# Kernel optimization log

Measured on AMD Instinct MI355X. Metric: run time of the kernel, lower is better.

The kernel has to match this reference:

```python
import jax, jax.numpy as jnp
import numpy as np

D = 8        # input_path_dim
S = 64       # cde_state_dim
H = 128      # vf_hidden_dim
OUT = 8      # output_path_dim
T = 2049     # time samples
B = 32       # batch (vmapped)
WIN = 16     # signature_window_size
NWIN = (T - 1) // WIN   # 128 scan steps
II, JJ = np.triu_indices(D, 1)    # Lyndon words of length 2: pairs i<j (P=28)


def setup_inputs() -> dict:
    key = jax.random.key(0)
    ks = jax.random.split(key, 16)
    g = lambda k, shp, fan: (jax.random.normal(k, shp, dtype=jnp.float32) / np.sqrt(fan)).astype(jnp.float32)
    z = lambda n: jnp.zeros((n,), jnp.float32)
    return {
        "ts": jnp.arange(T, dtype=jnp.float32),
        "x": jax.random.normal(ks[0], (B, T, D), dtype=jnp.float32) * 0.1,
        # initial MLP: d -> H -> H -> S, softplus activations
        "Wi0": g(ks[1], (H, D), D), "bi0": z(H),
        "Wi1": g(ks[2], (H, H), H), "bi1": z(H),
        "Wi2": g(ks[3], (S, H), H), "bi2": z(S),
        # vector-field MLP: S -> H -> H -> D*S, softplus hidden, tanh final
        "Wv0": g(ks[4], (H, S), S), "bv0": z(H),
        "Wv1": g(ks[5], (H, H), H), "bv1": z(H),
        "Wv2": g(ks[6], (D * S, H), H), "bv2": z(D * S),
        # readout: S -> OUT
        "Wr": g(ks[7], (OUT, S), S), "br": z(OUT),
    }


def _logsignatures(x):
    """Depth-2 log-signatures of a piecewise-linear path over windows.
    x: (B, T, D). Returns s1: (B, NWIN, D) increments, s2: (B, NWIN, P) Levy areas
    in the Lyndon basis [e_i, e_j], i<j."""
    delta = x[:, 1:] - x[:, :-1]                      # (B, T-1, D)
    delta = delta[:, : NWIN * WIN].reshape(x.shape[0], NWIN, WIN, D)
    s1 = delta.sum(axis=2)                            # (B, NWIN, D)
    cum = jnp.cumsum(delta, axis=2) - delta           # exclusive prefix sums
    M = jnp.einsum("bnwi,bnwj->bnij", cum, delta)    # (B, NWIN, D, D)
    L = 0.5 * (M - jnp.swapaxes(M, -1, -2))           # antisymmetric Levy area
    s2 = L[..., II, JJ]                               # (B, NWIN, P)
    return s1, s2


def reference(ts, x, Wi0, bi0, Wi1, bi1, Wi2, bi2, Wv0, bv0, Wv1, bv1, Wv2, bv2, Wr, br):
    sp = jax.nn.softplus

    def initial(x0):  # (D,) -> (S,)
        z = sp(Wi0 @ x0 + bi0)
        z = sp(Wi1 @ z + bi1)
        return Wi2 @ z + bi2

    def vf(h):  # (S,) -> (D, S): one vector field per input channel
        z = sp(Wv0 @ h + bv0)
        z = sp(Wv1 @ z + bv1)
        return jnp.tanh(Wv2 @ z + bv2).reshape(D, S)

    s1, s2 = _logsignatures(x)

    def single(x0_s, s1_s, s2_s):
        h0 = initial(x0_s)

        def step(h, sig):
            a, b = sig  # depth-1 (D,), depth-2 Lyndon coeffs (P,)
            V = vf(h)                          # (D, S)
            J = jax.jacfwd(vf)(h)              # (D, S, S) Jacobians dV_i/dh
            JV = jnp.einsum("dab,eb->dea", J, V)   # JV[j,i] = J_j @ V_i
            brack = JV[JJ, II] - JV[II, JJ]        # (P, S): [V_i, V_j], i<j
            hn = h + a @ V + b @ brack             # log-ODE step
            return hn, hn

        _, hist = jax.lax.scan(step, h0, (s1_s, s2_s))
        return jnp.concatenate([h0[None], hist], axis=0)   # (NWIN+1, S)

    hist = jax.vmap(single)(x[:, 0], s1, s2)    # (B, NWIN+1, S)
    return jnp.einsum("bns,os->bno", hist, Wr) + br   # evolving readout, identity act
```

## Files before the change

### kernel.cpp

```cpp
#include <hip/hip_runtime.h>
#include <hip/hip_bf16.h>

#define DD 8
#define SS 64
#define HH 128
#define OUTD 8
#define TT 2049
#define BB 32
#define WINW 16
#define NWIN 128
#define PP 28

typedef __attribute__((ext_vector_type(8))) short short8v;
typedef __attribute__((ext_vector_type(4))) float f32x4;

__device__ __forceinline__ float softplus_f(float x){
    return fmaxf(x, 0.f) + __logf(1.f + __expf(-fabsf(x)));
}
__device__ __forceinline__ float tanh_f(float x){
    float e = __expf(2.f * x);
    return 1.f - 2.f / (e + 1.f);
}
__device__ __forceinline__ void sp_sig(float x, float& sp, float& sg){
    float t = __expf(-fabsf(x));
    float r = 1.f / (1.f + t);
    sg = x > 0.f ? r : 1.f - r;
    sp = fmaxf(x, 0.f) - __logf(r);
}
__device__ __forceinline__ unsigned short f2bf(float f){
    return __builtin_bit_cast(unsigned short, __float2bfloat16(f));
}
__device__ __forceinline__ unsigned pk2(float a, float b){
    unsigned lo = (unsigned)__builtin_bit_cast(unsigned short, __float2bfloat16(a));
    unsigned hi = (unsigned)__builtin_bit_cast(unsigned short, __float2bfloat16(b));
    return lo | (hi << 16);
}

__global__ void sig_kernel(const float* __restrict__ x,
                           float* __restrict__ s1o, float* __restrict__ s2o){
    int w = blockIdx.x * blockDim.x + threadIdx.x;
    if (w >= BB * NWIN) return;
    int b = w >> 7, n = w & (NWIN - 1);
    const float* xp = x + ((size_t)b * TT + (size_t)n * WINW) * DD;
    float prev[DD], cum[DD], s1v[DD], M[DD][DD];
    #pragma unroll
    for (int i = 0; i < DD; ++i){
        cum[i] = 0.f; s1v[i] = 0.f;
        #pragma unroll
        for (int j = 0; j < DD; ++j) M[i][j] = 0.f;
    }
    #pragma unroll
    for (int i = 0; i < DD; ++i) prev[i] = xp[i];
    for (int t = 0; t < WINW; ++t){
        float cur[DD], del[DD];
        #pragma unroll
        for (int i = 0; i < DD; ++i) cur[i] = xp[(t + 1) * DD + i];
        #pragma unroll
        for (int i = 0; i < DD; ++i) del[i] = cur[i] - prev[i];
        #pragma unroll
        for (int i = 0; i < DD; ++i){
            #pragma unroll
            for (int j = 0; j < DD; ++j) M[i][j] += cum[i] * del[j];
        }
        #pragma unroll
        for (int i = 0; i < DD; ++i){ cum[i] += del[i]; s1v[i] += del[i]; prev[i] = cur[i]; }
    }
    #pragma unroll
    for (int i = 0; i < DD; ++i) s1o[(size_t)w * DD + i] = s1v[i];
    int p = 0;
    #pragma unroll
    for (int i = 0; i < DD; ++i){
        #pragma unroll
        for (int j = i + 1; j < DD; ++j){ s2o[(size_t)w * PP + p] = 0.5f * (M[i][j] - M[j][i]); ++p; }
    }
}

#define BPOS(k, nn) ((((k) >> 5) * 64 + (((k) >> 3) & 3) * 16 + (nn)) * 8 + ((k) & 7))

__global__ __launch_bounds__(512, 2) void scan_kernel(
    const float* __restrict__ x,
    const float* __restrict__ Wi0, const float* __restrict__ bi0,
    const float* __restrict__ Wi1, const float* __restrict__ bi1,
    const float* __restrict__ Wi2, const float* __restrict__ bi2,
    const float* __restrict__ Wv0, const float* __restrict__ bv0,
    const float* __restrict__ Wv1, const float* __restrict__ bv1,
    const float* __restrict__ Wv2, const float* __restrict__ bv2,
    const float* __restrict__ Wr,  const float* __restrict__ br,
    const float* __restrict__ s1g, const float* __restrict__ s2g,
    float* __restrict__ out)
{
    const int tid = threadIdx.x;
    const int w   = tid >> 6;
    const int l   = tid & 63;
    const int lg  = l >> 4;
    const int ln  = l & 15;
    const int b0  = blockIdx.x * 4;

    __shared__ __align__(16) short BpH[2 * 64 * 8];
    __shared__ __align__(16) short Bp0[4 * 64 * 8];
    __shared__ __align__(16) short Bp1[4 * 64 * 8];
    __shared__ __align__(16) short Bp7[2][2 * 64 * 8];
    __shared__ __align__(16) short Bp8[2][4 * 64 * 8];
    __shared__ __align__(16) short Bp9[2][4 * 64 * 8];
    __shared__ __align__(16) float s0p[4][HH], s1p[4][HH];
    __shared__ __align__(16) float Vl[4 * 512], Rf[4 * 512];
    __shared__ __align__(16) float hfb[4][2][SS];
    __shared__ __align__(16) float bv0L[HH], bv1L[HH], bv2L[512];
    __shared__ __align__(16) float WrL[OUTD * SS];
    __shared__ float brL[OUTD];
    __shared__ __align__(16) float sAll[4][NWIN * DD];
    __shared__ __align__(16) float bAll[4][NWIN * PP];
    __shared__ __align__(16) float outC[4][32][OUTD];
    __shared__ __align__(16) float Cexp[4][DD][12];

    short8v a0f[2], a1f[4];
    short8v a2f0[4], a2f1[4], a2f2[4], a2f3[4];
    #pragma unroll
    for (int ks = 0; ks < 2; ++ks){
        const float* p = Wv0 + (size_t)(w * 16 + ln) * SS + ks * 32 + lg * 8;
        short8v f;
        #pragma unroll
        for (int j = 0; j < 8; ++j) f[j] = (short)f2bf(p[j]);
        a0f[ks] = f;
    }
    #pragma unroll
    for (int ks = 0; ks < 4; ++ks){
        const float* p = Wv1 + (size_t)(w * 16 + ln) * HH + ks * 32 + lg * 8;
        short8v f;
        #pragma unroll
        for (int j = 0; j < 8; ++j) f[j] = (short)f2bf(p[j]);
        a1f[ks] = f;
    }
    #pragma unroll
    for (int ks = 0; ks < 4; ++ks){
        const float* p0 = Wv2 + (size_t)(64 * w + 0 * 16 + ln) * HH + ks * 32 + lg * 8;
        const float* p1 = Wv2 + (size_t)(64 * w + 1 * 16 + ln) * HH + ks * 32 + lg * 8;
        const float* p2 = Wv2 + (size_t)(64 * w + 2 * 16 + ln) * HH + ks * 32 + lg * 8;
        const float* p3 = Wv2 + (size_t)(64 * w + 3 * 16 + ln) * HH + ks * 32 + lg * 8;
        short8v f0, f1, f2, f3;
        #pragma unroll
        for (int j = 0; j < 8; ++j){
            f0[j] = (short)f2bf(p0[j]); f1[j] = (short)f2bf(p1[j]);
            f2[j] = (short)f2bf(p2[j]); f3[j] = (short)f2bf(p3[j]);
        }
        a2f0[ks] = f0; a2f1[ks] = f1; a2f2[ks] = f2; a2f3[ks] = f3;
    }
    if (tid < HH){ bv0L[tid] = bv0[tid]; bv1L[tid] = bv1[tid]; }
    bv2L[tid] = bv2[tid];
    WrL[tid]  = Wr[tid];
    if (tid < OUTD) brL[tid] = br[tid];
    {
        float* sF = &sAll[0][0];
        for (int i = tid; i < 4 * NWIN * DD; i += 512){
            int c = i >> 10;
            sF[i] = s1g[(size_t)(b0 + c) * (NWIN * DD) + (i & 1023)];
        }
        float* bF = &bAll[0][0];
        for (int i = tid; i < 4 * NWIN * PP; i += 512){
            int c = i / (NWIN * PP);
            bF[i] = s2g[(size_t)(b0 + c) * (NWIN * PP) + (i - c * (NWIN * PP))];
        }
        for (int i = tid; i < 2 * 64 * 8; i += 512) BpH[i] = 0;
        for (int i = tid; i < 4 * 64 * 8; i += 512){ Bp0[i] = 0; Bp1[i] = 0; }
    }
    __syncthreads();

    {
        int c4 = tid >> 7, r = tid & 127;
        float acc = bi0[r];
        const float* x0 = x + (size_t)(b0 + c4) * TT * DD;
        #pragma unroll
        for (int k = 0; k < DD; ++k) acc += Wi0[r * DD + k] * x0[k];
        s0p[c4][r] = softplus_f(acc);
    }
    if (tid < 256){
        int cc = tid >> 6, dd = (tid >> 3) & 7, ee = tid & 7;
        const float* bco = &bAll[cc][0];
        float cv = 0.f;
        if (ee < dd)      cv =  bco[((ee * (15 - ee)) >> 1) + dd - ee - 1];
        else if (ee > dd) cv = -bco[((dd * (15 - dd)) >> 1) + ee - dd - 1];
        Cexp[cc][dd][ee] = cv;
    }
    __syncthreads();
    {
        int c4 = tid >> 7, r = tid & 127;
        float acc = bi1[r];
        const f32x4* wv = (const f32x4*)(Wi1 + (size_t)r * HH);
        const f32x4* zv = (const f32x4*)&s0p[c4][0];
        #pragma unroll 8
        for (int k = 0; k < 32; ++k){
            f32x4 a = wv[k], z = zv[k];
            acc += a.x * z.x + a.y * z.y + a.z * z.z + a.w * z.w;
        }
        s1p[c4][r] = softplus_f(acc);
    }
    __syncthreads();
    if (tid < 256){
        int c4 = tid >> 6, s = tid & 63;
        float acc = bi2[s];
        const f32x4* wv = (const f32x4*)(Wi2 + (size_t)s * HH);
        const f32x4* zv = (const f32x4*)&s1p[c4][0];
        #pragma unroll 8
        for (int k = 0; k < 32; ++k){
            f32x4 a = wv[k], z = zv[k];
            acc += a.x * z.x + a.y * z.y + a.z * z.z + a.w * z.w;
        }
        hfb[c4][0][s] = acc;
        BpH[BPOS(s, c4)] = (short)f2bf(acc);
    }
    __syncthreads();

    const f32x4 zero4 = {0.f, 0.f, 0.f, 0.f};
    const int rb = w * 16 + lg * 4;

    for (int n = 0; n < NWIN; ++n){
        {
            f32x4 acc = zero4;
            acc = __builtin_amdgcn_mfma_f32_16x16x32_bf16(a0f[0], *(const short8v*)&BpH[(0 * 64 + l) * 8], acc, 0, 0, 0);
            acc = __builtin_amdgcn_mfma_f32_16x16x32_bf16(a0f[1], *(const short8v*)&BpH[(1 * 64 + l) * 8], acc, 0, 0, 0);
            if (ln < 4){
                int c = ln;
                f32x4 bv = *(const f32x4*)&bv0L[rb];
                float z[4], sgv[4];
                #pragma unroll
                for (int r = 0; r < 4; ++r){
                    float zz, gg;
                    sp_sig(acc[r] + bv[r], zz, gg);
                    z[r] = zz; sgv[r] = gg;
                }
                f32x4 sg = {sgv[0], sgv[1], sgv[2], sgv[3]};
                *(f32x4*)&s0p[c][rb] = sg;
                uint2 pk; pk.x = pk2(z[0], z[1]); pk.y = pk2(z[2], z[3]);
                *(uint2*)&Bp0[BPOS(rb, c)] = pk;
            }
        }
        __syncthreads();

        {
            f32x4 acc = zero4;
            #pragma unroll
            for (int ks = 0; ks < 4; ++ks)
                acc = __builtin_amdgcn_mfma_f32_16x16x32_bf16(a1f[ks], *(const short8v*)&Bp0[(ks * 64 + l) * 8], acc, 0, 0, 0);
            if (ln < 4){
                int c = ln;
                f32x4 bv = *(const f32x4*)&bv1L[rb];
                float z[4], sgv[4];
                #pragma unroll
                for (int r = 0; r < 4; ++r){
                    float zz, gg;
                    sp_sig(acc[r] + bv[r], zz, gg);
                    z[r] = zz; sgv[r] = gg;
                }
                f32x4 sg = {sgv[0], sgv[1], sgv[2], sgv[3]};
                *(f32x4*)&s1p[c][rb] = sg;
                uint2 pk; pk.x = pk2(z[0], z[1]); pk.y = pk2(z[2], z[3]);
                #pragma unroll
                for (int cc = 0; cc < 4; ++cc) *(uint2*)&Bp1[BPOS(rb, c * 4 + cc)] = pk;
            }
        }
        __syncthreads();

        {
            short8v bf[4];
            #pragma unroll
            for (int ks = 0; ks < 4; ++ks) bf[ks] = *(const short8v*)&Bp1[(ks * 64 + l) * 8];
            f32x4 acc0 = zero4, acc1 = zero4, acc2 = zero4, acc3 = zero4;
            #pragma unroll
            for (int ks = 0; ks < 4; ++ks){
                acc0 = __builtin_amdgcn_mfma_f32_16x16x32_bf16(a2f0[ks], bf[ks], acc0, 0, 0, 0);
                acc1 = __builtin_amdgcn_mfma_f32_16x16x32_bf16(a2f1[ks], bf[ks], acc1, 0, 0, 0);
                acc2 = __builtin_amdgcn_mfma_f32_16x16x32_bf16(a2f2[ks], bf[ks], acc2, 0, 0, 0);
                acc3 = __builtin_amdgcn_mfma_f32_16x16x32_bf16(a2f3[ks], bf[ks], acc3, 0, 0, 0);
            }
            {
                int c = ln >> 2, t = ln & 3;
                f32x4 av = (t == 0) ? acc0 : (t == 1) ? acc1 : (t == 2) ? acc2 : acc3;
                int r4 = 64 * w + t * 16 + lg * 4;
                f32x4 bv = *(const f32x4*)&bv2L[r4];
                f32x4 vv;
                #pragma unroll
                for (int r = 0; r < 4; ++r) vv[r] = tanh_f(av[r] + bv[r]);
                *(f32x4*)&Vl[c * 512 + r4] = vv;
            }
        }
        __syncthreads();

        {
            int c = tid >> 7, d = (tid >> 4) & 7, s0v = (tid & 15) * 4;
            f32x4 cm0 = *(const f32x4*)&Cexp[c][d][0];
            f32x4 cm1 = *(const f32x4*)&Cexp[c][d][4];
            f32x4 acc = zero4;
            #pragma unroll
            for (int e = 0; e < 8; ++e){
                float ce = (e < 4) ? cm0[e] : cm1[e - 4];
                f32x4 v4 = *(const f32x4*)&Vl[c * 512 + e * 64 + s0v];
                acc.x += ce * v4.x; acc.y += ce * v4.y;
                acc.z += ce * v4.z; acc.w += ce * v4.w;
            }
            uint2 pk; pk.x = pk2(acc.x, acc.y); pk.y = pk2(acc.z, acc.w);
            *(uint2*)&Bp7[c >> 1][BPOS(s0v, (c & 1) * 8 + d)] = pk;
        }
        __syncthreads();

        {
            #pragma unroll
            for (int p = 0; p < 2; ++p){
                f32x4 acc = zero4;
                acc = __builtin_amdgcn_mfma_f32_16x16x32_bf16(a0f[0], *(const short8v*)&Bp7[p][(0 * 64 + l) * 8], acc, 0, 0, 0);
                acc = __builtin_amdgcn_mfma_f32_16x16x32_bf16(a0f[1], *(const short8v*)&Bp7[p][(1 * 64 + l) * 8], acc, 0, 0, 0);
                int c = 2 * p + (ln >> 3);
                f32x4 sg = *(const f32x4*)&s0p[c][rb];
                uint2 pk; pk.x = pk2(sg[0] * acc[0], sg[1] * acc[1]);
                pk.y = pk2(sg[2] * acc[2], sg[3] * acc[3]);
                *(uint2*)&Bp8[p][BPOS(rb, ln)] = pk;
            }
        }
        __syncthreads();

        {
            #pragma unroll
            for (int p = 0; p < 2; ++p){
                f32x4 acc = zero4;
                #pragma unroll
                for (int ks = 0; ks < 4; ++ks)
                    acc = __builtin_amdgcn_mfma_f32_16x16x32_bf16(a1f[ks], *(const short8v*)&Bp8[p][(ks * 64 + l) * 8], acc, 0, 0, 0);
                int c = 2 * p + (ln >> 3), d = ln & 7;
                f32x4 sg = *(const f32x4*)&s1p[c][rb];
                uint2 pk; pk.x = pk2(sg[0] * acc[0], sg[1] * acc[1]);
                pk.y = pk2(sg[2] * acc[2], sg[3] * acc[3]);
                *(uint2*)&Bp9[d >> 2][BPOS(rb, (d & 3) * 4 + c)] = pk;
            }
        }
        __syncthreads();

        {
            const int im = w >> 2;
            short8v bf[4];
            #pragma unroll
            for (int ks = 0; ks < 4; ++ks) bf[ks] = *(const short8v*)&Bp9[im][(ks * 64 + l) * 8];
            f32x4 acc0 = zero4, acc1 = zero4, acc2 = zero4, acc3 = zero4;
            #pragma unroll
            for (int ks = 0; ks < 4; ++ks){
                acc0 = __builtin_amdgcn_mfma_f32_16x16x32_bf16(a2f0[ks], bf[ks], acc0, 0, 0, 0);
                acc1 = __builtin_amdgcn_mfma_f32_16x16x32_bf16(a2f1[ks], bf[ks], acc1, 0, 0, 0);
                acc2 = __builtin_amdgcn_mfma_f32_16x16x32_bf16(a2f2[ks], bf[ks], acc2, 0, 0, 0);
                acc3 = __builtin_amdgcn_mfma_f32_16x16x32_bf16(a2f3[ks], bf[ks], acc3, 0, 0, 0);
            }
            if ((ln >> 2) == (w & 3)){
                int c = ln & 3;
                #pragma unroll
                for (int t = 0; t < 4; ++t){
                    f32x4 av = (t == 0) ? acc0 : (t == 1) ? acc1 : (t == 2) ? acc2 : acc3;
                    int r4 = 64 * w + t * 16 + lg * 4;
                    f32x4 vv = *(const f32x4*)&Vl[c * 512 + r4];
                    f32x4 rr;
                    #pragma unroll
                    for (int r = 0; r < 4; ++r) rr[r] = (1.f - vv[r] * vv[r]) * av[r];
                    *(f32x4*)&Rf[c * 512 + r4] = rr;
                }
            }
        }
        __syncthreads();

        {
            const int cur = n & 1;
            if (w < 4){
                int c = w, s = l;
                f32x4 a0 = *(const f32x4*)&sAll[c][n * DD];
                f32x4 a1 = *(const f32x4*)&sAll[c][n * DD + 4];
                float hN = hfb[c][cur][s];
                #pragma unroll
                for (int d = 0; d < 4; ++d)
                    hN += a0[d] * Vl[c * 512 + d * 64 + s] + Rf[c * 512 + d * 64 + s];
                #pragma unroll
                for (int d = 4; d < 8; ++d)
                    hN += a1[d - 4] * Vl[c * 512 + d * 64 + s] + Rf[c * 512 + d * 64 + s];
                hfb[c][cur ^ 1][s] = hN;
                BpH[BPOS(s, c)] = (short)f2bf(hN);
            } else {
                {
                    int idx = (w - 4) * 64 + l;
                    int cc = idx >> 6, dd = (idx >> 3) & 7, ee = idx & 7;
                    int nn = (n + 1 < NWIN) ? n + 1 : NWIN - 1;
                    const float* bco = &bAll[cc][nn * PP];
                    float cv = 0.f;
                    if (ee < dd)      cv =  bco[((ee * (15 - ee)) >> 1) + dd - ee - 1];
                    else if (ee > dd) cv = -bco[((dd * (15 - dd)) >> 1) + ee - dd - 1];
                    Cexp[cc][dd][ee] = cv;
                }
                int c = w - 4;
                int o = l >> 3, qq = l & 7;
                f32x4 w0 = *(const f32x4*)&WrL[o * SS + qq * 8];
                f32x4 w1 = *(const f32x4*)&WrL[o * SS + qq * 8 + 4];
                f32x4 h0 = *(const f32x4*)&hfb[c][cur][qq * 8];
                f32x4 h1 = *(const f32x4*)&hfb[c][cur][qq * 8 + 4];
                float acc = w0.x*h0.x + w0.y*h0.y + w0.z*h0.z + w0.w*h0.w
                          + w1.x*h1.x + w1.y*h1.y + w1.z*h1.z + w1.w*h1.w;
                acc += __shfl_xor(acc, 1); acc += __shfl_xor(acc, 2); acc += __shfl_xor(acc, 4);
                if (qq == 0) outC[c][n & 31][o] = brL[o] + acc;
                if ((n & 31) == 31){
                    size_t base = (size_t)(b0 + c) * (NWIN + 1) * OUTD + (size_t)(n - 31) * OUTD;
                    const f32x4* oc = (const f32x4*)&outC[c][0][0];
                    f32x4 v = oc[l];
                    *(f32x4*)&out[base + l * 4] = v;
                }
            }
        }
        __syncthreads();
    }

    if (w >= 4){
        int c = w - 4;
        int o = l >> 3, qq = l & 7;
        f32x4 w0 = *(const f32x4*)&WrL[o * SS + qq * 8];
        f32x4 w1 = *(const f32x4*)&WrL[o * SS + qq * 8 + 4];
        f32x4 h0 = *(const f32x4*)&hfb[c][0][qq * 8];
        f32x4 h1 = *(const f32x4*)&hfb[c][0][qq * 8 + 4];
        float acc = w0.x*h0.x + w0.y*h0.y + w0.z*h0.z + w0.w*h0.w
                  + w1.x*h1.x + w1.y*h1.y + w1.z*h1.z + w1.w*h1.w;
        acc += __shfl_xor(acc, 1); acc += __shfl_xor(acc, 2); acc += __shfl_xor(acc, 4);
        if (qq == 0)
            out[(size_t)(b0 + c) * (NWIN + 1) * OUTD + (size_t)NWIN * OUTD + o] = brL[o] + acc;
    }
}

extern "C" void kernel_launch(void* const* d_in, const int* in_sizes, int n_in,
                              void* d_out, int out_size, void* d_ws, size_t ws_size,
                              hipStream_t stream){
    const float* x   = (const float*)d_in[1];
    const float* Wi0 = (const float*)d_in[2];
    const float* bi0 = (const float*)d_in[3];
    const float* Wi1 = (const float*)d_in[4];
    const float* bi1 = (const float*)d_in[5];
    const float* Wi2 = (const float*)d_in[6];
    const float* bi2 = (const float*)d_in[7];
    const float* Wv0 = (const float*)d_in[8];
    const float* bv0 = (const float*)d_in[9];
    const float* Wv1 = (const float*)d_in[10];
    const float* bv1 = (const float*)d_in[11];
    const float* Wv2 = (const float*)d_in[12];
    const float* bv2 = (const float*)d_in[13];
    const float* Wr  = (const float*)d_in[14];
    const float* br  = (const float*)d_in[15];
    float* out = (float*)d_out;

    float* s1w = (float*)d_ws;
    float* s2w = s1w + (size_t)BB * NWIN * DD;

    sig_kernel<<<(BB * NWIN + 255) / 256, 256, 0, stream>>>(x, s1w, s2w);
    scan_kernel<<<BB / 4, 512, 0, stream>>>(x, Wi0, bi0, Wi1, bi1, Wi2, bi2,
                                            Wv0, bv0, Wv1, bv1, Wv2, bv2,
                                            Wr, br, s1w, s2w, out);
}
```

Baseline: 544.4 us.

## Process two batch samples per block instead of four, doubling grid size

Each block now handles 2 batch elements instead of 4, so 16 blocks run in place of 8. The Jacobian tangent MFMA stages shrink from two passes to one per step. The Cexp coefficient expansion is double-buffered so it overlaps with the bracket stage instead of the state-update stage, and the V/R buffers are padded to reduce LDS bank conflicts. More blocks use more CUs on a latency-bound sequential scan, but each MFMA now wastes more of its columns on padding.

```diff
diff --git a/kernel.cpp b/kernel.cpp
--- a/kernel.cpp
+++ b/kernel.cpp
@@ -10,6 +10,7 @@
 #define WINW 16
 #define NWIN 128
 #define PP 28
+#define VSTR 516
 
 typedef __attribute__((ext_vector_type(8))) short short8v;
 typedef __attribute__((ext_vector_type(4))) float f32x4;
@@ -94,24 +95,24 @@
     const int l   = tid & 63;
     const int lg  = l >> 4;
     const int ln  = l & 15;
-    const int b0  = blockIdx.x * 4;
+    const int b0  = blockIdx.x * 2;
 
     __shared__ __align__(16) short BpH[2 * 64 * 8];
     __shared__ __align__(16) short Bp0[4 * 64 * 8];
     __shared__ __align__(16) short Bp1[4 * 64 * 8];
-    __shared__ __align__(16) short Bp7[2][2 * 64 * 8];
-    __shared__ __align__(16) short Bp8[2][4 * 64 * 8];
-    __shared__ __align__(16) short Bp9[2][4 * 64 * 8];
-    __shared__ __align__(16) float s0p[4][HH], s1p[4][HH];
-    __shared__ __align__(16) float Vl[4 * 512], Rf[4 * 512];
-    __shared__ __align__(16) float hfb[4][2][SS];
+    __shared__ __align__(16) short Bp7[2 * 64 * 8];
+    __shared__ __align__(16) short Bp8[4 * 64 * 8];
+    __shared__ __align__(16) short Bp9[4 * 64 * 8];
+    __shared__ __align__(16) float s0p[2][HH], s1p[2][HH];
+    __shared__ __align__(16) float Vl[2 * VSTR], Rf[2 * VSTR];
+    __shared__ __align__(16) float hfb[2][2][SS];
     __shared__ __align__(16) float bv0L[HH], bv1L[HH], bv2L[512];
     __shared__ __align__(16) float WrL[OUTD * SS];
     __shared__ float brL[OUTD];
-    __shared__ __align__(16) float sAll[4][NWIN * DD];
-    __shared__ __align__(16) float bAll[4][NWIN * PP];
-    __shared__ __align__(16) float outC[4][32][OUTD];
-    __shared__ __align__(16) float Cexp[4][DD][12];
+    __shared__ __align__(16) float sAll[2][NWIN * DD];
+    __shared__ __align__(16) float bAll[2][NWIN * PP];
+    __shared__ __align__(16) float outC[2][32][OUTD];
+    __shared__ __align__(16) float Cexp[2][2][DD][12];
 
     short8v a0f[2], a1f[4];
     short8v a2f0[4], a2f1[4], a2f2[4], a2f3[4];
@@ -151,12 +152,12 @@
     if (tid < OUTD) brL[tid] = br[tid];
     {
         float* sF = &sAll[0][0];
-        for (int i = tid; i < 4 * NWIN * DD; i += 512){
+        for (int i = tid; i < 2 * NWIN * DD; i += 512){
             int c = i >> 10;
             sF[i] = s1g[(size_t)(b0 + c) * (NWIN * DD) + (i & 1023)];
         }
         float* bF = &bAll[0][0];
-        for (int i = tid; i < 4 * NWIN * PP; i += 512){
+        for (int i = tid; i < 2 * NWIN * PP; i += 512){
             int c = i / (NWIN * PP);
             bF[i] = s2g[(size_t)(b0 + c) * (NWIN * PP) + (i - c * (NWIN * PP))];
         }
@@ -165,24 +166,24 @@
     }
     __syncthreads();
 
-    {
+    if (tid < 256){
         int c4 = tid >> 7, r = tid & 127;
         float acc = bi0[r];
         const float* x0 = x + (size_t)(b0 + c4) * TT * DD;
         #pragma unroll
         for (int k = 0; k < DD; ++k) acc += Wi0[r * DD + k] * x0[k];
         s0p[c4][r] = softplus_f(acc);
-    }
-    if (tid < 256){
-        int cc = tid >> 6, dd = (tid >> 3) & 7, ee = tid & 7;
+    } else if (tid < 384){
+        int t2 = tid - 256;
+        int cc = t2 >> 6, dd = (t2 >> 3) & 7, ee = t2 & 7;
         const float* bco = &bAll[cc][0];
         float cv = 0.f;
         if (ee < dd)      cv =  bco[((ee * (15 - ee)) >> 1) + dd - ee - 1];
         else if (ee > dd) cv = -bco[((dd * (15 - dd)) >> 1) + ee - dd - 1];
-        Cexp[cc][dd][ee] = cv;
+        Cexp[0][cc][dd][ee] = cv;
     }
     __syncthreads();
-    {
+    if (tid < 256){
         int c4 = tid >> 7, r = tid & 127;
         float acc = bi1[r];
         const f32x4* wv = (const f32x4*)(Wi1 + (size_t)r * HH);
@@ -195,7 +196,7 @@
         s1p[c4][r] = softplus_f(acc);
     }
     __syncthreads();
-    if (tid < 256){
+    if (tid < 128){
         int c4 = tid >> 6, s = tid & 63;
         float acc = bi2[s];
         const f32x4* wv = (const f32x4*)(Wi2 + (size_t)s * HH);
@@ -214,11 +215,12 @@
     const int rb = w * 16 + lg * 4;
 
     for (int n = 0; n < NWIN; ++n){
+        const int cb = n & 1;
         {
             f32x4 acc = zero4;
             acc = __builtin_amdgcn_mfma_f32_16x16x32_bf16(a0f[0], *(const short8v*)&BpH[(0 * 64 + l) * 8], acc, 0, 0, 0);
             acc = __builtin_amdgcn_mfma_f32_16x16x32_bf16(a0f[1], *(const short8v*)&BpH[(1 * 64 + l) * 8], acc, 0, 0, 0);
-            if (ln < 4){
+            if (ln < 2){
                 int c = ln;
                 f32x4 bv = *(const f32x4*)&bv0L[rb];
                 float z[4], sgv[4];
@@ -241,7 +243,7 @@
             #pragma unroll
             for (int ks = 0; ks < 4; ++ks)
                 acc = __builtin_amdgcn_mfma_f32_16x16x32_bf16(a1f[ks], *(const short8v*)&Bp0[(ks * 64 + l) * 8], acc, 0, 0, 0);
-            if (ln < 4){
+            if (ln < 2){
                 int c = ln;
                 f32x4 bv = *(const f32x4*)&bv1L[rb];
                 float z[4], sgv[4];
@@ -272,7 +274,7 @@
                 acc2 = __builtin_amdgcn_mfma_f32_16x16x32_bf16(a2f2[ks], bf[ks], acc2, 0, 0, 0);
                 acc3 = __builtin_amdgcn_mfma_f32_16x16x32_bf16(a2f3[ks], bf[ks], acc3, 0, 0, 0);
             }
-            {
+            if (ln < 8){
                 int c = ln >> 2, t = ln & 3;
                 f32x4 av = (t == 0) ? acc0 : (t == 1) ? acc1 : (t == 2) ? acc2 : acc3;
                 int r4 = 64 * w + t * 16 + lg * 4;
@@ -280,64 +282,68 @@
                 f32x4 vv;
                 #pragma unroll
                 for (int r = 0; r < 4; ++r) vv[r] = tanh_f(av[r] + bv[r]);
-                *(f32x4*)&Vl[c * 512 + r4] = vv;
-            }
-        }
-        __syncthreads();
-
-        {
-            int c = tid >> 7, d = (tid >> 4) & 7, s0v = (tid & 15) * 4;
-            f32x4 cm0 = *(const f32x4*)&Cexp[c][d][0];
-            f32x4 cm1 = *(const f32x4*)&Cexp[c][d][4];
+                *(f32x4*)&Vl[c * VSTR + r4] = vv;
+            }
+        }
+        __syncthreads();
+
+        {
+            if (tid < 256){
+                int c = tid >> 7, d = (tid >> 4) & 7, s0v = (tid & 15) * 4;
+                f32x4 cm0 = *(const f32x4*)&Cexp[cb][c][d][0];
+                f32x4 cm1 = *(const f32x4*)&Cexp[cb][c][d][4];
+                f32x4 acc = zero4;
+                #pragma unroll
+                for (int e = 0; e < 8; ++e){
+                    float ce = (e < 4) ? cm0[e] : cm1[e - 4];
+                    f32x4 v4 = *(const f32x4*)&Vl[c * VSTR + e * 64 + s0v];
+                    acc.x += ce * v4.x; acc.y += ce * v4.y;
+                    acc.z += ce * v4.z; acc.w += ce * v4.w;
+                }
+                uint2 pk; pk.x = pk2(acc.x, acc.y); pk.y = pk2(acc.z, acc.w);
+                *(uint2*)&Bp7[BPOS(s0v, c * 8 + d)] = pk;
+            } else if (tid < 384){
+                int idx = tid - 256;
+                int cc = idx >> 6, dd = (idx >> 3) & 7, ee = idx & 7;
+                int nn = (n + 1 < NWIN) ? n + 1 : NWIN - 1;
+                const float* bco = &bAll[cc][nn * PP];
+                float cv = 0.f;
+                if (ee < dd)      cv =  bco[((ee * (15 - ee)) >> 1) + dd - ee - 1];
+                else if (ee > dd) cv = -bco[((dd * (15 - dd)) >> 1) + ee - dd - 1];
+                Cexp[cb ^ 1][cc][dd][ee] = cv;
+            }
+        }
+        __syncthreads();
+
+        {
             f32x4 acc = zero4;
-            #pragma unroll
-            for (int e = 0; e < 8; ++e){
-                float ce = (e < 4) ? cm0[e] : cm1[e - 4];
-                f32x4 v4 = *(const f32x4*)&Vl[c * 512 + e * 64 + s0v];
-                acc.x += ce * v4.x; acc.y += ce * v4.y;
-                acc.z += ce * v4.z; acc.w += ce * v4.w;
-            }
-            uint2 pk; pk.x = pk2(acc.x, acc.y); pk.y = pk2(acc.z, acc.w);
-            *(uint2*)&Bp7[c >> 1][BPOS(s0v, (c & 1) * 8 + d)] = pk;
-        }
-        __syncthreads();
-
-        {
-            #pragma unroll
-            for (int p = 0; p < 2; ++p){
-                f32x4 acc = zero4;
-                acc = __builtin_amdgcn_mfma_f32_16x16x32_bf16(a0f[0], *(const short8v*)&Bp7[p][(0 * 64 + l) * 8], acc, 0, 0, 0);
-                acc = __builtin_amdgcn_mfma_f32_16x16x32_bf16(a0f[1], *(const short8v*)&Bp7[p][(1 * 64 + l) * 8], acc, 0, 0, 0);
-                int c = 2 * p + (ln >> 3);
-                f32x4 sg = *(const f32x4*)&s0p[c][rb];
-                uint2 pk; pk.x = pk2(sg[0] * acc[0], sg[1] * acc[1]);
-                pk.y = pk2(sg[2] * acc[2], sg[3] * acc[3]);
-                *(uint2*)&Bp8[p][BPOS(rb, ln)] = pk;
-            }
-        }
-        __syncthreads();
-
-        {
-            #pragma unroll
-            for (int p = 0; p < 2; ++p){
-                f32x4 acc = zero4;
-                #pragma unroll
-                for (int ks = 0; ks < 4; ++ks)
-                    acc = __builtin_amdgcn_mfma_f32_16x16x32_bf16(a1f[ks], *(const short8v*)&Bp8[p][(ks * 64 + l) * 8], acc, 0, 0, 0);
-                int c = 2 * p + (ln >> 3), d = ln & 7;
-                f32x4 sg = *(const f32x4*)&s1p[c][rb];
-                uint2 pk; pk.x = pk2(sg[0] * acc[0], sg[1] * acc[1]);
-                pk.y = pk2(sg[2] * acc[2], sg[3] * acc[3]);
-                *(uint2*)&Bp9[d >> 2][BPOS(rb, (d & 3) * 4 + c)] = pk;
-            }
-        }
-        __syncthreads();
-
-        {
-            const int im = w >> 2;
+            acc = __builtin_amdgcn_mfma_f32_16x16x32_bf16(a0f[0], *(const short8v*)&Bp7[(0 * 64 + l) * 8], acc, 0, 0, 0);
+            acc = __builtin_amdgcn_mfma_f32_16x16x32_bf16(a0f[1], *(const short8v*)&Bp7[(1 * 64 + l) * 8], acc, 0, 0, 0);
+            int c = ln >> 3;
+            f32x4 sg = *(const f32x4*)&s0p[c][rb];
+            uint2 pk; pk.x = pk2(sg[0] * acc[0], sg[1] * acc[1]);
+            pk.y = pk2(sg[2] * acc[2], sg[3] * acc[3]);
+            *(uint2*)&Bp8[BPOS(rb, ln)] = pk;
+        }
+        __syncthreads();
+
+        {
+            f32x4 acc = zero4;
+            #pragma unroll
+            for (int ks = 0; ks < 4; ++ks)
+                acc = __builtin_amdgcn_mfma_f32_16x16x32_bf16(a1f[ks], *(const short8v*)&Bp8[(ks * 64 + l) * 8], acc, 0, 0, 0);
+            int c = ln >> 3;
+            f32x4 sg = *(const f32x4*)&s1p[c][rb];
+            uint2 pk; pk.x = pk2(sg[0] * acc[0], sg[1] * acc[1]);
+            pk.y = pk2(sg[2] * acc[2], sg[3] * acc[3]);
+            *(uint2*)&Bp9[BPOS(rb, ln)] = pk;
+        }
+        __syncthreads();
+
+        {
             short8v bf[4];
             #pragma unroll
-            for (int ks = 0; ks < 4; ++ks) bf[ks] = *(const short8v*)&Bp9[im][(ks * 64 + l) * 8];
+            for (int ks = 0; ks < 4; ++ks) bf[ks] = *(const short8v*)&Bp9[(ks * 64 + l) * 8];
             f32x4 acc0 = zero4, acc1 = zero4, acc2 = zero4, acc3 = zero4;
             #pragma unroll
             for (int ks = 0; ks < 4; ++ks){
@@ -346,17 +352,17 @@
                 acc2 = __builtin_amdgcn_mfma_f32_16x16x32_bf16(a2f2[ks], bf[ks], acc2, 0, 0, 0);
                 acc3 = __builtin_amdgcn_mfma_f32_16x16x32_bf16(a2f3[ks], bf[ks], acc3, 0, 0, 0);
             }
-            if ((ln >> 2) == (w & 3)){
-                int c = ln & 3;
+            if ((ln & 7) == w){
+                int c = ln >> 3;
                 #pragma unroll
                 for (int t = 0; t < 4; ++t){
                     f32x4 av = (t == 0) ? acc0 : (t == 1) ? acc1 : (t == 2) ? acc2 : acc3;
                     int r4 = 64 * w + t * 16 + lg * 4;
-                    f32x4 vv = *(const f32x4*)&Vl[c * 512 + r4];
+                    f32x4 vv = *(const f32x4*)&Vl[c * VSTR + r4];
                     f32x4 rr;
                     #pragma unroll
                     for (int r = 0; r < 4; ++r) rr[r] = (1.f - vv[r] * vv[r]) * av[r];
-                    *(f32x4*)&Rf[c * 512 + r4] = rr;
+                    *(f32x4*)&Rf[c * VSTR + r4] = rr;
                 }
             }
         }
@@ -364,31 +370,21 @@
 
         {
             const int cur = n & 1;
-            if (w < 4){
+            if (w < 2){
                 int c = w, s = l;
                 f32x4 a0 = *(const f32x4*)&sAll[c][n * DD];
                 f32x4 a1 = *(const f32x4*)&sAll[c][n * DD + 4];
                 float hN = hfb[c][cur][s];
                 #pragma unroll
                 for (int d = 0; d < 4; ++d)
-                    hN += a0[d] * Vl[c * 512 + d * 64 + s] + Rf[c * 512 + d * 64 + s];
+                    hN += a0[d] * Vl[c * VSTR + d * 64 + s] + Rf[c * VSTR + d * 64 + s];
                 #pragma unroll
                 for (int d = 4; d < 8; ++d)
-                    hN += a1[d - 4] * Vl[c * 512 + d * 64 + s] + Rf[c * 512 + d * 64 + s];
+                    hN += a1[d - 4] * Vl[c * VSTR + d * 64 + s] + Rf[c * VSTR + d * 64 + s];
                 hfb[c][cur ^ 1][s] = hN;
                 BpH[BPOS(s, c)] = (short)f2bf(hN);
-            } else {
-                {
-                    int idx = (w - 4) * 64 + l;
-                    int cc = idx >> 6, dd = (idx >> 3) & 7, ee = idx & 7;
-                    int nn = (n + 1 < NWIN) ? n + 1 : NWIN - 1;
-                    const float* bco = &bAll[cc][nn * PP];
-                    float cv = 0.f;
-                    if (ee < dd)      cv =  bco[((ee * (15 - ee)) >> 1) + dd - ee - 1];
-                    else if (ee > dd) cv = -bco[((dd * (15 - dd)) >> 1) + ee - dd - 1];
-                    Cexp[cc][dd][ee] = cv;
-                }
-                int c = w - 4;
+            } else if (w < 4){
+                int c = w - 2;
                 int o = l >> 3, qq = l & 7;
                 f32x4 w0 = *(const f32x4*)&WrL[o * SS + qq * 8];
                 f32x4 w1 = *(const f32x4*)&WrL[o * SS + qq * 8 + 4];
@@ -409,8 +405,8 @@
         __syncthreads();
     }
 
-    if (w >= 4){
-        int c = w - 4;
+    if (w == 2 || w == 3){
+        int c = w - 2;
         int o = l >> 3, qq = l & 7;
         f32x4 w0 = *(const f32x4*)&WrL[o * SS + qq * 8];
         f32x4 w1 = *(const f32x4*)&WrL[o * SS + qq * 8 + 4];
@@ -448,7 +444,7 @@
     float* s2w = s1w + (size_t)BB * NWIN * DD;
 
     sig_kernel<<<(BB * NWIN + 255) / 256, 256, 0, stream>>>(x, s1w, s2w);
-    scan_kernel<<<BB / 4, 512, 0, stream>>>(x, Wi0, bi0, Wi1, bi1, Wi2, bi2,
+    scan_kernel<<<BB / 2, 512, 0, stream>>>(x, Wi0, bi0, Wi1, bi1, Wi2, bi2,
                                             Wv0, bv0, Wv1, bv1, Wv2, bv2,
                                             Wr, br, s1w, s2w, out);
 }
```

Result: slower. 651.8 us (+19.7%).

## Permute Wv2 rows so the state update fuses into the Jacobian GEMM epilogue

Applied to the files above, without the earlier changes.

Reorders the Wv2 MFMA A-fragments so each wave owns a group of state indices across all input channels, not a block of output rows. This lets the final Jacobian-vector MFMA compute both Bp9 halves and reduce over channels with lane shuffles, applying the h update directly. That removes the Rf buffer and one block-wide barrier per scan step. The readout and next-step Cexp construction move into the earlier bracket-coefficient phase, using a double-buffered Cexp and padded Vl strides. The cost is doubled MFMA work per wave in the last GEMM plus extra shuffles.

```diff
diff --git a/kernel.cpp b/kernel.cpp
--- a/kernel.cpp
+++ b/kernel.cpp
@@ -10,6 +10,8 @@
 #define WINW 16
 #define NWIN 128
 #define PP 28
+#define DSTR 68
+#define CSTR 548
 
 typedef __attribute__((ext_vector_type(8))) short short8v;
 typedef __attribute__((ext_vector_type(4))) float f32x4;
@@ -103,7 +105,7 @@
     __shared__ __align__(16) short Bp8[2][4 * 64 * 8];
     __shared__ __align__(16) short Bp9[2][4 * 64 * 8];
     __shared__ __align__(16) float s0p[4][HH], s1p[4][HH];
-    __shared__ __align__(16) float Vl[4 * 512], Rf[4 * 512];
+    __shared__ __align__(16) float Vl[4 * CSTR];
     __shared__ __align__(16) float hfb[4][2][SS];
     __shared__ __align__(16) float bv0L[HH], bv1L[HH], bv2L[512];
     __shared__ __align__(16) float WrL[OUTD * SS];
@@ -111,10 +113,10 @@
     __shared__ __align__(16) float sAll[4][NWIN * DD];
     __shared__ __align__(16) float bAll[4][NWIN * PP];
     __shared__ __align__(16) float outC[4][32][OUTD];
-    __shared__ __align__(16) float Cexp[4][DD][12];
+    __shared__ __align__(16) float Cexp[2][4][DD][12];
 
     short8v a0f[2], a1f[4];
-    short8v a2f0[4], a2f1[4], a2f2[4], a2f3[4];
+    short8v a2p0[4], a2p1[4], a2p2[4], a2p3[4];
     #pragma unroll
     for (int ks = 0; ks < 2; ++ks){
         const float* p = Wv0 + (size_t)(w * 16 + ln) * SS + ks * 32 + lg * 8;
@@ -131,19 +133,24 @@
         for (int j = 0; j < 8; ++j) f[j] = (short)f2bf(p[j]);
         a1f[ks] = f;
     }
-    #pragma unroll
-    for (int ks = 0; ks < 4; ++ks){
-        const float* p0 = Wv2 + (size_t)(64 * w + 0 * 16 + ln) * HH + ks * 32 + lg * 8;
-        const float* p1 = Wv2 + (size_t)(64 * w + 1 * 16 + ln) * HH + ks * 32 + lg * 8;
-        const float* p2 = Wv2 + (size_t)(64 * w + 2 * 16 + ln) * HH + ks * 32 + lg * 8;
-        const float* p3 = Wv2 + (size_t)(64 * w + 3 * 16 + ln) * HH + ks * 32 + lg * 8;
-        short8v f0, f1, f2, f3;
-        #pragma unroll
-        for (int j = 0; j < 8; ++j){
-            f0[j] = (short)f2bf(p0[j]); f1[j] = (short)f2bf(p1[j]);
-            f2[j] = (short)f2bf(p2[j]); f3[j] = (short)f2bf(p3[j]);
-        }
-        a2f0[ks] = f0; a2f1[ks] = f1; a2f2[ks] = f2; a2f3[ks] = f3;
+    {
+        const int dP = ln & 7;
+        #pragma unroll
+        for (int t = 0; t < 4; ++t){
+            const int sP = 8 * w + 2 * t + (ln >> 3);
+            const float* p = Wv2 + (size_t)(dP * 64 + sP) * HH;
+            #pragma unroll
+            for (int ks = 0; ks < 4; ++ks){
+                const float* pp = p + ks * 32 + lg * 8;
+                short8v f;
+                #pragma unroll
+                for (int j = 0; j < 8; ++j) f[j] = (short)f2bf(pp[j]);
+                if (t == 0) a2p0[ks] = f;
+                else if (t == 1) a2p1[ks] = f;
+                else if (t == 2) a2p2[ks] = f;
+                else a2p3[ks] = f;
+            }
+        }
     }
     if (tid < HH){ bv0L[tid] = bv0[tid]; bv1L[tid] = bv1[tid]; }
     bv2L[tid] = bv2[tid];
@@ -179,7 +186,7 @@
         float cv = 0.f;
         if (ee < dd)      cv =  bco[((ee * (15 - ee)) >> 1) + dd - ee - 1];
         else if (ee > dd) cv = -bco[((dd * (15 - dd)) >> 1) + ee - dd - 1];
-        Cexp[cc][dd][ee] = cv;
+        Cexp[0][cc][dd][ee] = cv;
     }
     __syncthreads();
     {
@@ -214,6 +221,7 @@
     const int rb = w * 16 + lg * 4;
 
     for (int n = 0; n < NWIN; ++n){
+        const int cur = n & 1;
         {
             f32x4 acc = zero4;
             acc = __builtin_amdgcn_mfma_f32_16x16x32_bf16(a0f[0], *(const short8v*)&BpH[(0 * 64 + l) * 8], acc, 0, 0, 0);
@@ -267,38 +275,82 @@
             f32x4 acc0 = zero4, acc1 = zero4, acc2 = zero4, acc3 = zero4;
             #pragma unroll
             for (int ks = 0; ks < 4; ++ks){
-                acc0 = __builtin_amdgcn_mfma_f32_16x16x32_bf16(a2f0[ks], bf[ks], acc0, 0, 0, 0);
-                acc1 = __builtin_amdgcn_mfma_f32_16x16x32_bf16(a2f1[ks], bf[ks], acc1, 0, 0, 0);
-                acc2 = __builtin_amdgcn_mfma_f32_16x16x32_bf16(a2f2[ks], bf[ks], acc2, 0, 0, 0);
-                acc3 = __builtin_amdgcn_mfma_f32_16x16x32_bf16(a2f3[ks], bf[ks], acc3, 0, 0, 0);
+                acc0 = __builtin_amdgcn_mfma_f32_16x16x32_bf16(a2p0[ks], bf[ks], acc0, 0, 0, 0);
+                acc1 = __builtin_amdgcn_mfma_f32_16x16x32_bf16(a2p1[ks], bf[ks], acc1, 0, 0, 0);
+                acc2 = __builtin_amdgcn_mfma_f32_16x16x32_bf16(a2p2[ks], bf[ks], acc2, 0, 0, 0);
+                acc3 = __builtin_amdgcn_mfma_f32_16x16x32_bf16(a2p3[ks], bf[ks], acc3, 0, 0, 0);
             }
             {
-                int c = ln >> 2, t = ln & 3;
-                f32x4 av = (t == 0) ? acc0 : (t == 1) ? acc1 : (t == 2) ? acc2 : acc3;
-                int r4 = 64 * w + t * 16 + lg * 4;
-                f32x4 bv = *(const f32x4*)&bv2L[r4];
-                f32x4 vv;
-                #pragma unroll
-                for (int r = 0; r < 4; ++r) vv[r] = tanh_f(av[r] + bv[r]);
-                *(f32x4*)&Vl[c * 512 + r4] = vv;
-            }
-        }
-        __syncthreads();
-
-        {
-            int c = tid >> 7, d = (tid >> 4) & 7, s0v = (tid & 15) * 4;
-            f32x4 cm0 = *(const f32x4*)&Cexp[c][d][0];
-            f32x4 cm1 = *(const f32x4*)&Cexp[c][d][4];
-            f32x4 acc = zero4;
-            #pragma unroll
-            for (int e = 0; e < 8; ++e){
-                float ce = (e < 4) ? cm0[e] : cm1[e - 4];
-                f32x4 v4 = *(const f32x4*)&Vl[c * 512 + e * 64 + s0v];
-                acc.x += ce * v4.x; acc.y += ce * v4.y;
-                acc.z += ce * v4.z; acc.w += ce * v4.w;
-            }
-            uint2 pk; pk.x = pk2(acc.x, acc.y); pk.y = pk2(acc.z, acc.w);
-            *(uint2*)&Bp7[c >> 1][BPOS(s0v, (c & 1) * 8 + d)] = pk;
+                int c = ln >> 2, rs = ln & 3;
+                int d = (lg & 1) * 4 + rs, b = lg >> 1;
+                #pragma unroll
+                for (int t = 0; t < 4; ++t){
+                    int s = 8 * w + 2 * t + b;
+                    float av = (t == 0) ? acc0[rs] : (t == 1) ? acc1[rs] : (t == 2) ? acc2[rs] : acc3[rs];
+                    float v = tanh_f(av + bv2L[d * 64 + s]);
+                    Vl[c * CSTR + d * DSTR + s] = v;
+                }
+            }
+        }
+        __syncthreads();
+
+        {
+            if (tid < 256){
+                int c = tid >> 6, d = (tid >> 3) & 7, s0 = (tid & 7) * 8;
+                f32x4 cm0 = *(const f32x4*)&Cexp[cur][c][d][0];
+                f32x4 cm1 = *(const f32x4*)&Cexp[cur][c][d][4];
+                #pragma unroll
+                for (int qq = 0; qq < 2; ++qq){
+                    int sv = s0 + qq * 4;
+                    f32x4 acc = zero4;
+                    #pragma unroll
+                    for (int e = 0; e < 8; ++e){
+                        float ce = (e < 4) ? cm0[e] : cm1[e - 4];
+                        f32x4 v4 = *(const f32x4*)&Vl[c * CSTR + e * DSTR + sv];
+                        acc.x += ce * v4.x; acc.y += ce * v4.y;
+                        acc.z += ce * v4.z; acc.w += ce * v4.w;
+                    }
+                    uint2 pk; pk.x = pk2(acc.x, acc.y); pk.y = pk2(acc.z, acc.w);
+                    *(uint2*)&Bp7[c >> 1][BPOS(sv, (c & 1) * 8 + d)] = pk;
+                }
+            } else if (tid < 384){
+                int idx = tid - 256;
+                int cc = idx >> 5, dd = (idx >> 2) & 7, ep = idx & 3;
+                int nn = (n + 1 < NWIN) ? n + 1 : NWIN - 1;
+                const float* bco = &bAll[cc][nn * PP];
+                #pragma unroll
+                for (int h2 = 0; h2 < 2; ++h2){
+                    int ee = ep + h2 * 4;
+                    float cv = 0.f;
+                    if (ee < dd)      cv =  bco[((ee * (15 - ee)) >> 1) + dd - ee - 1];
+                    else if (ee > dd) cv = -bco[((dd * (15 - dd)) >> 1) + ee - dd - 1];
+                    Cexp[cur ^ 1][cc][dd][ee] = cv;
+                }
+            } else {
+                int lh = l & 31;
+                int c2 = ((tid >> 6) - 6) * 2 + (l >> 5);
+                int o = (lh >> 2) & 7, q2 = lh & 3;
+                float acc = 0.f;
+                #pragma unroll
+                for (int i = 0; i < 4; ++i){
+                    f32x4 wv = *(const f32x4*)&WrL[o * SS + q2 * 16 + i * 4];
+                    f32x4 hv = *(const f32x4*)&hfb[c2][cur][q2 * 16 + i * 4];
+                    acc += wv.x * hv.x + wv.y * hv.y + wv.z * hv.z + wv.w * hv.w;
+                }
+                acc += __shfl_xor(acc, 1); acc += __shfl_xor(acc, 2);
+                if (q2 == 0) outC[c2][n & 31][o] = brL[o] + acc;
+                if ((n & 31) == 31){
+                    int lid = (tid - 384);
+                    #pragma unroll
+                    for (int k = 0; k < 2; ++k){
+                        int slot = lid * 2 + k;
+                        int c = slot >> 6, rem = slot & 63;
+                        size_t base = (size_t)(b0 + c) * (NWIN + 1) * OUTD + (size_t)(n - 31) * OUTD;
+                        const f32x4* oc = (const f32x4*)&outC[c][0][0];
+                        *(f32x4*)&out[base + rem * 4] = oc[rem];
+                    }
+                }
+            }
         }
         __syncthreads();
 
@@ -334,93 +386,69 @@
         __syncthreads();
 
         {
-            const int im = w >> 2;
-            short8v bf[4];
-            #pragma unroll
-            for (int ks = 0; ks < 4; ++ks) bf[ks] = *(const short8v*)&Bp9[im][(ks * 64 + l) * 8];
-            f32x4 acc0 = zero4, acc1 = zero4, acc2 = zero4, acc3 = zero4;
-            #pragma unroll
-            for (int ks = 0; ks < 4; ++ks){
-                acc0 = __builtin_amdgcn_mfma_f32_16x16x32_bf16(a2f0[ks], bf[ks], acc0, 0, 0, 0);
-                acc1 = __builtin_amdgcn_mfma_f32_16x16x32_bf16(a2f1[ks], bf[ks], acc1, 0, 0, 0);
-                acc2 = __builtin_amdgcn_mfma_f32_16x16x32_bf16(a2f2[ks], bf[ks], acc2, 0, 0, 0);
-                acc3 = __builtin_amdgcn_mfma_f32_16x16x32_bf16(a2f3[ks], bf[ks], acc3, 0, 0, 0);
-            }
-            if ((ln >> 2) == (w & 3)){
-                int c = ln & 3;
+            f32x4 accA[2][4];
+            #pragma unroll
+            for (int p = 0; p < 2; ++p){
+                short8v bf[4];
+                #pragma unroll
+                for (int ks = 0; ks < 4; ++ks) bf[ks] = *(const short8v*)&Bp9[p][(ks * 64 + l) * 8];
+                f32x4 t0a = zero4, t1a = zero4, t2a = zero4, t3a = zero4;
+                #pragma unroll
+                for (int ks = 0; ks < 4; ++ks){
+                    t0a = __builtin_amdgcn_mfma_f32_16x16x32_bf16(a2p0[ks], bf[ks], t0a, 0, 0, 0);
+                    t1a = __builtin_amdgcn_mfma_f32_16x16x32_bf16(a2p1[ks], bf[ks], t1a, 0, 0, 0);
+                    t2a = __builtin_amdgcn_mfma_f32_16x16x32_bf16(a2p2[ks], bf[ks], t2a, 0, 0, 0);
+                    t3a = __builtin_amdgcn_mfma_f32_16x16x32_bf16(a2p3[ks], bf[ks], t3a, 0, 0, 0);
+                }
+                accA[p][0] = t0a; accA[p][1] = t1a; accA[p][2] = t2a; accA[p][3] = t3a;
+            }
+            const int p  = lg & 1;
+            const int rs = ln >> 2;
+            const int c  = ln & 3;
+            const int d  = p * 4 + rs;
+            const int b  = lg >> 1;
+            const float aval = sAll[c][n * DD + d];
+            float P[4];
+            #pragma unroll
+            for (int t = 0; t < 4; ++t){
+                int s = 8 * w + 2 * t + b;
+                float v = Vl[c * CSTR + d * DSTR + s];
+                float pre = accA[p][t][rs];
+                P[t] = (1.f - v * v) * pre + aval * v;
+            }
+            #pragma unroll
+            for (int t = 0; t < 4; ++t){
+                P[t] += __shfl_xor(P[t], 4);
+                P[t] += __shfl_xor(P[t], 8);
+                P[t] += __shfl_xor(P[t], 16);
+            }
+            if (p == 0 && rs == 0){
                 #pragma unroll
                 for (int t = 0; t < 4; ++t){
-                    f32x4 av = (t == 0) ? acc0 : (t == 1) ? acc1 : (t == 2) ? acc2 : acc3;
-                    int r4 = 64 * w + t * 16 + lg * 4;
-                    f32x4 vv = *(const f32x4*)&Vl[c * 512 + r4];
-                    f32x4 rr;
-                    #pragma unroll
-                    for (int r = 0; r < 4; ++r) rr[r] = (1.f - vv[r] * vv[r]) * av[r];
-                    *(f32x4*)&Rf[c * 512 + r4] = rr;
-                }
-            }
-        }
-        __syncthreads();
-
-        {
-            const int cur = n & 1;
-            if (w < 4){
-                int c = w, s = l;
-                f32x4 a0 = *(const f32x4*)&sAll[c][n * DD];
-                f32x4 a1 = *(const f32x4*)&sAll[c][n * DD + 4];
-                float hN = hfb[c][cur][s];
-                #pragma unroll
-                for (int d = 0; d < 4; ++d)
-                    hN += a0[d] * Vl[c * 512 + d * 64 + s] + Rf[c * 512 + d * 64 + s];
-                #pragma unroll
-                for (int d = 4; d < 8; ++d)
-                    hN += a1[d - 4] * Vl[c * 512 + d * 64 + s] + Rf[c * 512 + d * 64 + s];
-                hfb[c][cur ^ 1][s] = hN;
-                BpH[BPOS(s, c)] = (short)f2bf(hN);
-            } else {
-                {
-                    int idx = (w - 4) * 64 + l;
-                    int cc = idx >> 6, dd = (idx >> 3) & 7, ee = idx & 7;
-                    int nn = (n + 1 < NWIN) ? n + 1 : NWIN - 1;
-                    const float* bco = &bAll[cc][nn * PP];
-                    float cv = 0.f;
-                    if (ee < dd)      cv =  bco[((ee * (15 - ee)) >> 1) + dd - ee - 1];
-                    else if (ee > dd) cv = -bco[((dd * (15 - dd)) >> 1) + ee - dd - 1];
-                    Cexp[cc][dd][ee] = cv;
-                }
-                int c = w - 4;
-                int o = l >> 3, qq = l & 7;
-                f32x4 w0 = *(const f32x4*)&WrL[o * SS + qq * 8];
-                f32x4 w1 = *(const f32x4*)&WrL[o * SS + qq * 8 + 4];
-                f32x4 h0 = *(const f32x4*)&hfb[c][cur][qq * 8];
-                f32x4 h1 = *(const f32x4*)&hfb[c][cur][qq * 8 + 4];
-                float acc = w0.x*h0.x + w0.y*h0.y + w0.z*h0.z + w0.w*h0.w
-                          + w1.x*h1.x + w1.y*h1.y + w1.z*h1.z + w1.w*h1.w;
-                acc += __shfl_xor(acc, 1); acc += __shfl_xor(acc, 2); acc += __shfl_xor(acc, 4);
-                if (qq == 0) outC[c][n & 31][o] = brL[o] + acc;
-                if ((n & 31) == 31){
-                    size_t base = (size_t)(b0 + c) * (NWIN + 1) * OUTD + (size_t)(n - 31) * OUTD;
-                    const f32x4* oc = (const f32x4*)&outC[c][0][0];
-                    f32x4 v = oc[l];
-                    *(f32x4*)&out[base + l * 4] = v;
-                }
-            }
-        }
-        __syncthreads();
-    }
-
-    if (w >= 4){
-        int c = w - 4;
-        int o = l >> 3, qq = l & 7;
-        f32x4 w0 = *(const f32x4*)&WrL[o * SS + qq * 8];
-        f32x4 w1 = *(const f32x4*)&WrL[o * SS + qq * 8 + 4];
-        f32x4 h0 = *(const f32x4*)&hfb[c][0][qq * 8];
-        f32x4 h1 = *(const f32x4*)&hfb[c][0][qq * 8 + 4];
-        float acc = w0.x*h0.x + w0.y*h0.y + w0.z*h0.z + w0.w*h0.w
-                  + w1.x*h1.x + w1.y*h1.y + w1.z*h1.z + w1.w*h1.w;
-        acc += __shfl_xor(acc, 1); acc += __shfl_xor(acc, 2); acc += __shfl_xor(acc, 4);
-        if (qq == 0)
-            out[(size_t)(b0 + c) * (NWIN + 1) * OUTD + (size_t)NWIN * OUTD + o] = brL[o] + acc;
+                    int s = 8 * w + 2 * t + b;
+                    float hN = hfb[c][cur][s] + P[t];
+                    hfb[c][cur ^ 1][s] = hN;
+                    BpH[BPOS(s, c)] = (short)f2bf(hN);
+                }
+            }
+        }
+        __syncthreads();
+    }
+
+    if (tid >= 384){
+        int lh = l & 31;
+        int c2 = ((tid >> 6) - 6) * 2 + (l >> 5);
+        int o = (lh >> 2) & 7, q2 = lh & 3;
+        float acc = 0.f;
+        #pragma unroll
+        for (int i = 0; i < 4; ++i){
+            f32x4 wv = *(const f32x4*)&WrL[o * SS + q2 * 16 + i * 4];
+            f32x4 hv = *(const f32x4*)&hfb[c2][0][q2 * 16 + i * 4];
+            acc += wv.x * hv.x + wv.y * hv.y + wv.z * hv.z + wv.w * hv.w;
+        }
+        acc += __shfl_xor(acc, 1); acc += __shfl_xor(acc, 2);
+        if (q2 == 0)
+            out[(size_t)(b0 + c2) * (NWIN + 1) * OUTD + (size_t)NWIN * OUTD + o] = brL[o] + acc;
     }
 }
 
```

Result: slower. 964.1 us (+77.1%).
